# Optimization experiments

Hardware: AMD Instinct MI355X
Metric: run time of the kernel (lower is better)

The kernel has to match this reference:

```python
import jax, jax.numpy as jnp
import numpy as np

N_NODES = 100000
N_EDGES = 1600000
N_GRAPHS = 2000
N_FEAT = 128
HIDDEN = 128
N_LAYERS = 4
BN_EPS = 1e-5


def setup_inputs() -> dict:
    key = jax.random.key(0)
    ks = jax.random.split(key, 8)
    x = jax.random.normal(ks[0], (N_NODES, N_FEAT), dtype=jnp.float32)
    edge_index = jax.random.randint(ks[1], (2, N_EDGES), 0, N_NODES, dtype=jnp.int32)
    batch = jnp.sort(jax.random.randint(ks[2], (N_NODES,), 0, N_GRAPHS, dtype=jnp.int32))
    # layer weights scaled down to keep activations stable over 4 layers
    Ws = jax.random.normal(ks[3], (N_LAYERS, HIDDEN, HIDDEN), dtype=jnp.float32) * 0.1
    bs = jnp.zeros((N_LAYERS, HIDDEN), jnp.float32)
    gammas = jnp.ones((N_LAYERS, HIDDEN), jnp.float32)
    betas = jnp.zeros((N_LAYERS, HIDDEN), jnp.float32)
    run_mean = jnp.zeros((N_LAYERS, HIDDEN), jnp.float32)
    run_var = jnp.ones((N_LAYERS, HIDDEN), jnp.float32)
    W_out = jax.random.normal(ks[4], (HIDDEN, 5), dtype=jnp.float32) * 0.1
    b_out = jnp.zeros((5,), jnp.float32)
    return {"x": x, "edge_index": edge_index, "batch": batch, "Ws": Ws, "bs": bs,
            "gammas": gammas, "betas": betas, "run_mean": run_mean, "run_var": run_var,
            "W_out": W_out, "b_out": b_out}


def _gcn_conv(x, src, dst, norm, self_coef, W, b):
    xw = x @ W                                        # [N, H]
    coef = norm[src] * norm[dst]                      # [E]
    msgs = xw[src] * coef[:, None]                    # [E, H] gather
    agg = jax.ops.segment_sum(msgs, dst, num_segments=N_NODES)  # scatter-add
    agg = agg + xw * self_coef[:, None]               # self-loop term
    return agg + b


def reference(x, edge_index, batch, Ws, bs, gammas, betas, run_mean, run_var, W_out, b_out):
    src, dst = edge_index[0], edge_index[1]
    # degree (incl. self-loop) from destination index
    deg = jax.ops.segment_sum(jnp.ones((N_EDGES,), x.dtype), dst, num_segments=N_NODES) + 1.0
    norm = jax.lax.rsqrt(deg)
    self_coef = norm * norm
    h = x
    for l in range(N_LAYERS):
        h = _gcn_conv(h, src, dst, norm, self_coef, Ws[l], bs[l])
        # BatchNorm1d in eval mode (running stats); dropout is identity in eval
        h = (h - run_mean[l]) * (gammas[l] * jax.lax.rsqrt(run_var[l] + BN_EPS)) + betas[l]
        h = jax.nn.relu(h)
    # global mean pool over graphs
    sums = jax.ops.segment_sum(h, batch, num_segments=N_GRAPHS)
    counts = jax.ops.segment_sum(jnp.ones((N_NODES,), h.dtype), batch, num_segments=N_GRAPHS)
    pooled = sums / jnp.maximum(counts, 1.0)[:, None]  # [G, H]
    return pooled @ W_out + b_out                      # [G, 5]
```

## Files before the change

kernel.cpp:

```cpp
#include <hip/hip_runtime.h>
#include <hip/hip_fp16.h>

#define N_NODES_C 100000
#define N_EDGES_C 1600000
#define N_GRAPHS_C 2000
#define HID 128
#define BN_EPS_C 1e-5f
#define NBUCK 391
#define PART_TILE 4096

typedef _Float16 half8 __attribute__((ext_vector_type(8)));
typedef float float4v __attribute__((ext_vector_type(4)));


__global__ __launch_bounds__(256) void k_twhist(const float* __restrict__ Ws_all, _Float16* __restrict__ WT,
                                                const int* __restrict__ dst, int* __restrict__ bcount,
                                                _Float16* __restrict__ yB_dummy) {
    const int t = threadIdx.x;
    int idx = blockIdx.x * 256 + t;
    if (idx < 4 * HID * HID) {
        int l = idx >> 14, r = idx & 16383, k = r >> 7, n = r & 127;
        WT[l * 16384 + n * HID + k] = (_Float16)Ws_all[idx];
    }
    if (blockIdx.x == 390 && t < 64) ((int*)yB_dummy)[t] = 0;
    __shared__ int hist[NBUCK];
    for (int b = t; b < NBUCK; b += 256) hist[b] = 0;
    __syncthreads();
    const int e0 = blockIdx.x * PART_TILE;
    #pragma unroll
    for (int k = 0; k < 16; k++) {
        int e = e0 + k * 256 + t;
        if (e < N_EDGES_C) atomicAdd(&hist[dst[e] >> 8], 1);
    }
    __syncthreads();
    for (int b = t; b < NBUCK; b += 256) {
        int c = hist[b];
        if (c) atomicAdd(&bcount[b], c);
    }
}

__global__ __launch_bounds__(256) void kb_part(const int* __restrict__ src, const int* __restrict__ dst,
                                               const int* __restrict__ bcount, int* __restrict__ relcur,
                                               int* __restrict__ ebuf) {
    __shared__ int sb[512];
    __shared__ int hist[NBUCK];
    __shared__ int startA[NBUCK];
    __shared__ int lcur[NBUCK];
    const int t = threadIdx.x;
    int v0 = (t < NBUCK) ? bcount[t] : 0;
    int v1 = (t + 256 < NBUCK) ? bcount[t + 256] : 0;
    sb[t] = v0; sb[t + 256] = v1;
    for (int b = t; b < NBUCK; b += 256) { hist[b] = 0; lcur[b] = 0; }
    __syncthreads();
    for (int off = 1; off < 512; off <<= 1) {
        int a  = (t >= off) ? sb[t - off] : 0;
        int b2 = (t + 256 >= off) ? sb[t + 256 - off] : 0;
        __syncthreads();
        sb[t] += a; sb[t + 256] += b2;
        __syncthreads();
    }
    sb[t] -= v0; sb[t + 256] -= v1;
    __syncthreads();
    const int e0 = blockIdx.x * PART_TILE;
    #pragma unroll
    for (int k = 0; k < 16; k++) {
        int e = e0 + k * 256 + t;
        if (e < N_EDGES_C) atomicAdd(&hist[dst[e] >> 8], 1);
    }
    __syncthreads();
    for (int b = t; b < NBUCK; b += 256) {
        int c = hist[b];
        startA[b] = c ? (sb[b] + atomicAdd(&relcur[b], c)) : 0;
    }
    __syncthreads();
    #pragma unroll
    for (int k = 0; k < 16; k++) {
        int e = e0 + k * 256 + t;
        if (e < N_EDGES_C) {
            int d = dst[e];
            int b = d >> 8;
            int pos = startA[b] + atomicAdd(&lcur[b], 1);
            ebuf[pos] = (src[e] << 8) | (d & 255);
        }
    }
}

__global__ __launch_bounds__(256) void kb_fill(const int* __restrict__ ebuf, const int* __restrict__ bcount,
                                               int* __restrict__ csr_src, int* __restrict__ offs,
                                               float* __restrict__ norm) {
    __shared__ int sb[512];
    __shared__ int s[256];
    __shared__ int excl[256];
    __shared__ int lcur[256];
    const int b = blockIdx.x, t = threadIdx.x;
    int v0 = (t < NBUCK) ? bcount[t] : 0;
    int v1 = (t + 256 < NBUCK) ? bcount[t + 256] : 0;
    sb[t] = v0; sb[t + 256] = v1;
    s[t] = 0; lcur[t] = 0;
    __syncthreads();
    for (int off = 1; off < 512; off <<= 1) {
        int a  = (t >= off) ? sb[t - off] : 0;
        int b2 = (t + 256 >= off) ? sb[t + 256 - off] : 0;
        __syncthreads();
        sb[t] += a; sb[t + 256] += b2;
        __syncthreads();
    }
    sb[t] -= v0; sb[t + 256] -= v1;
    __syncthreads();
    const int base = b << 8;
    const int e0 = sb[b], e1 = sb[b] + bcount[b];
    for (int e = e0 + t; e < e1; e += 256)
        atomicAdd(&s[ebuf[e] & 255], 1);
    __syncthreads();
    int own = s[t];
    for (int off = 1; off < 256; off <<= 1) {
        int v = (t >= off) ? s[t - off] : 0;
        __syncthreads();
        s[t] += v;
        __syncthreads();
    }
    excl[t] = s[t] - own;
    int node = base + t;
    if (node < N_NODES_C) {
        offs[node] = e0 + (s[t] - own);
        norm[node] = rsqrtf((float)own + 1.0f);
    }
    if (b == 0 && t == 0) offs[N_NODES_C] = N_EDGES_C;
    __syncthreads();
    for (int e = e0 + t; e < e1; e += 256) {
        int p = ebuf[e];
        int l = p & 255;
        int pos = e0 + excl[l] + atomicAdd(&lcur[l], 1);
        csr_src[pos] = p >> 8;
    }
}


__global__ __launch_bounds__(256) void k_gemm0(const float* __restrict__ Ap,
                                               const _Float16* __restrict__ WT,
                                               const float* __restrict__ norm,
                                               _Float16* __restrict__ Y, int nrows) {
    __shared__ _Float16 Wt[HID][136];
    const int tid = threadIdx.x;
    #pragma unroll
    for (int t = 0; t < 8; t++) {
        int off = tid * 8 + t * 2048;
        *(half8*)&Wt[off >> 7][off & 127] = *(const half8*)&WT[off];
    }
    __syncthreads();

    const int wave = tid >> 6, lane = tid & 63, quad = lane >> 4, l16 = lane & 15;
    half8 Wf[2][4];
    #pragma unroll
    for (int c = 0; c < 2; c++)
        #pragma unroll
        for (int ks = 0; ks < 4; ks++)
            Wf[c][ks] = *(const half8*)&Wt[(wave * 2 + c) * 16 + l16][ks * 32 + quad * 8];

    const int nbase = blockIdx.x * 128;
    #pragma unroll
    for (int t = 0; t < 8; t++) {
        int node = nbase + t * 16 + l16;
        bool ok = node < nrows;
        half8 Af[4];
        const float* arow = Ap + (long)node * HID;
        #pragma unroll
        for (int ks = 0; ks < 4; ks++) {
            if (ok) {
                float4 fa = *(const float4*)&arow[ks * 32 + quad * 8];
                float4 fb = *(const float4*)&arow[ks * 32 + quad * 8 + 4];
                _Float16 pk[8] = {(_Float16)fa.x, (_Float16)fa.y, (_Float16)fa.z, (_Float16)fa.w,
                                  (_Float16)fb.x, (_Float16)fb.y, (_Float16)fb.z, (_Float16)fb.w};
                Af[ks] = *(half8*)pk;
            } else Af[ks] = half8{};
        }
        float4v a0 = {0.f, 0.f, 0.f, 0.f}, a1 = {0.f, 0.f, 0.f, 0.f};
        #pragma unroll
        for (int ks = 0; ks < 4; ks++) {
            a0 = __builtin_amdgcn_mfma_f32_16x16x32_f16(Wf[0][ks], Af[ks], a0, 0, 0, 0);
            a1 = __builtin_amdgcn_mfma_f32_16x16x32_f16(Wf[1][ks], Af[ks], a1, 0, 0, 0);
        }
        float nv = ok ? norm[node] : 0.f;
        _Float16 p0[4], p1[4];
        #pragma unroll
        for (int r = 0; r < 4; r++) {
            p0[r] = (_Float16)(a0[r] * nv);
            p1[r] = (_Float16)(a1[r] * nv);
        }
        *(ushort4*)&Y[(long)node * HID + (wave * 2 + 0) * 16 + quad * 4] = *(ushort4*)p0;
        *(ushort4*)&Y[(long)node * HID + (wave * 2 + 1) * 16 + quad * 4] = *(ushort4*)p1;
    }
}


template<bool LAST>
__global__ __launch_bounds__(512, 8) void k_fused(
    const __half* __restrict__ yin, _Float16* __restrict__ yout,
    const _Float16* __restrict__ WTn, const int* __restrict__ offs,
    const int* __restrict__ csr, const float* __restrict__ norm,
    const float* __restrict__ bias, const float* __restrict__ mean,
    const float* __restrict__ gam, const float* __restrict__ varr,
    const float* __restrict__ bet, const int* __restrict__ batch,
    float* __restrict__ psum, int* __restrict__ pcount)
{
    __shared__ __half ht[32][136];
    const int tid = threadIdx.x;
    const int wv = __builtin_amdgcn_readfirstlane(tid >> 6);
    const int lane = tid & 63;
    const int quad = lane >> 4, l16 = lane & 15;
    const int j = lane * 2;
    const int nbase = blockIdx.x * 32;

    half8 Wf[4];
    if constexpr (!LAST) {
        #pragma unroll
        for (int ks = 0; ks < 4; ks++)
            Wf[ks] = *(const half8*)&WTn[(long)(wv * 16 + l16) * HID + ks * 32 + quad * 8];
    }

    for (int r = 0; r < 4; r++) {
        const int li = wv * 4 + r;
        const int i = nbase + li;
        float2 f = __half22float2(*(const __half2*)&yin[(long)i * HID + j]);
        float acc0 = f.x, acc1 = f.y;
        const int e0 = offs[i], e1 = offs[i + 1];
        int e = e0;
        do {
            int id[16];
            #pragma unroll
            for (int u = 0; u < 16; u++) {
                int raw = csr[e + u];
                id[u] = (e + u < e1) ? raw : N_NODES_C;
            }
            #pragma unroll
            for (int u = 0; u < 16; u++) {
                float2 g2 = __half22float2(*(const __half2*)&yin[(long)id[u] * HID + j]);
                acc0 += g2.x; acc1 += g2.y;
            }
            e += 16;
        } while (e < e1);
        const float ni = norm[i];
        float2 bi = *(const float2*)&bias[j];
        float2 me = *(const float2*)&mean[j];
        float2 ga = *(const float2*)&gam[j];
        float2 va = *(const float2*)&varr[j];
        float2 be = *(const float2*)&bet[j];
        float v0 = (acc0 * ni + bi.x - me.x) * (ga.x * rsqrtf(va.x + BN_EPS_C)) + be.x;
        float v1 = (acc1 * ni + bi.y - me.y) * (ga.y * rsqrtf(va.y + BN_EPS_C)) + be.y;
        *(__half2*)&ht[li][j] = __floats2half2_rn(fmaxf(v0, 0.f), fmaxf(v1, 0.f));
    }
    __syncthreads();

    if constexpr (!LAST) {
        #pragma unroll
        for (int ng = 0; ng < 2; ng++) {
            half8 Af[4];
            #pragma unroll
            for (int ks = 0; ks < 4; ks++)
                Af[ks] = *(const half8*)&ht[ng * 16 + l16][ks * 32 + quad * 8];
            float4v a0 = {0.f, 0.f, 0.f, 0.f};
            #pragma unroll
            for (int ks = 0; ks < 4; ks++)
                a0 = __builtin_amdgcn_mfma_f32_16x16x32_f16(Wf[ks], Af[ks], a0, 0, 0, 0);
            const int node = nbase + ng * 16 + l16;
            const float nv = norm[node];
            _Float16 p[4];
            #pragma unroll
            for (int r = 0; r < 4; r++) p[r] = (_Float16)(a0[r] * nv);
            *(ushort4*)&yout[(long)node * HID + wv * 16 + quad * 4] = *(ushort4*)p;
        }
    } else {
        const int sub = tid >> 7, t7 = tid & 127;
        const int i0 = nbase + sub * 8, iend = i0 + 8;
        float acc = 0.f;
        int cur = batch[i0];
        int runStart = i0;
        for (int i = i0; i < iend; i++) {
            int g = batch[i];
            if (g != cur) {
                atomicAdd(&psum[(long)cur * HID + t7], acc);
                if (t7 == 0) atomicAdd(&pcount[cur], i - runStart);
                acc = 0.f; cur = g; runStart = i;
            }
            acc += __half2float(ht[i - nbase][t7]);
        }
        atomicAdd(&psum[(long)cur * HID + t7], acc);
        if (t7 == 0) atomicAdd(&pcount[cur], iend - runStart);
    }
}

__global__ __launch_bounds__(128) void k_final(const float* __restrict__ psum, const int* __restrict__ pcount,
                                               const float* __restrict__ W_out, const float* __restrict__ b_out,
                                               float* __restrict__ out) {
    __shared__ float red[128][5];
    const int g = blockIdx.x, j = threadIdx.x;
    float cnt = fmaxf((float)pcount[g], 1.f);
    float p = psum[(long)g * HID + j] / cnt;
    #pragma unroll
    for (int o = 0; o < 5; o++) red[j][o] = p * W_out[j * 5 + o];
    __syncthreads();
    for (int off = 64; off >= 1; off >>= 1) {
        if (j < off) {
            #pragma unroll
            for (int o = 0; o < 5; o++) red[j][o] += red[j + off][o];
        }
        __syncthreads();
    }
    if (j < 5) out[g * 5 + j] = red[0][j] + b_out[j];
}


extern "C" void kernel_launch(void* const* d_in, const int* in_sizes, int n_in,
                              void* d_out, int out_size, void* d_ws, size_t ws_size,
                              hipStream_t stream) {
    const float* x        = (const float*)d_in[0];
    const int*   eidx     = (const int*)d_in[1];
    const int*   src      = eidx;
    const int*   dst      = eidx + N_EDGES_C;
    const int*   batch    = (const int*)d_in[2];
    const float* Ws_all   = (const float*)d_in[3];
    const float* bs       = (const float*)d_in[4];
    const float* gammas   = (const float*)d_in[5];
    const float* betas    = (const float*)d_in[6];
    const float* run_mean = (const float*)d_in[7];
    const float* run_var  = (const float*)d_in[8];
    const float* W_out    = (const float*)d_in[9];
    const float* b_out    = (const float*)d_in[10];
    float* out = (float*)d_out;

    char* wp = (char*)d_ws;
    auto alloc = [&](size_t bytes) { char* p = wp; wp += (bytes + 255) & ~(size_t)255; return p; };
    _Float16* yA      = (_Float16*)alloc((size_t)(N_NODES_C + 128) * HID * 2);
    _Float16* yB      = (_Float16*)alloc((size_t)(N_NODES_C + 128) * HID * 2);
    int*      ebuf    = (int*)yA;
    _Float16* WT      = (_Float16*)alloc((size_t)4 * HID * HID * 2);
    int*      csr_src = (int*)alloc((size_t)(N_EDGES_C + 16) * 4);
    int*      offs    = (int*)alloc((size_t)(N_NODES_C + 1) * 4);
    float*    norm    = (float*)alloc((size_t)N_NODES_C * 4);
    char*     zbeg    = wp;
    float*    psum    = (float*)alloc((size_t)N_GRAPHS_C * HID * 4);
    int*      pcount  = (int*)alloc((size_t)N_GRAPHS_C * 4);
    int*      bcount  = (int*)alloc((NBUCK + 1) * 4);
    int*      relcur  = (int*)alloc((NBUCK + 1) * 4);
    size_t    zlen    = (size_t)(wp - zbeg);

    hipMemsetAsync(zbeg, 0, zlen, stream);

    const int PB = (N_EDGES_C + PART_TILE - 1) / PART_TILE;
    k_twhist<<<PB, 256, 0, stream>>>(Ws_all, WT, dst, bcount, yB + (size_t)N_NODES_C * HID);
    kb_part <<<PB, 256, 0, stream>>>(src, dst, bcount, relcur, ebuf);
    kb_fill <<<NBUCK, 256, 0, stream>>>(ebuf, bcount, csr_src, offs, norm);

    const int GB = (N_NODES_C + 127) / 128;
    const int FB = N_NODES_C / 32;
    k_gemm0<<<GB, 256, 0, stream>>>(x, WT, norm, yA, N_NODES_C);

    k_fused<false><<<FB, 512, 0, stream>>>((const __half*)yA, yB, WT + 1 * 16384, offs, csr_src, norm,
                                           bs + 0 * HID, run_mean + 0 * HID, gammas + 0 * HID,
                                           run_var + 0 * HID, betas + 0 * HID, nullptr, nullptr, nullptr);
    k_fused<false><<<FB, 512, 0, stream>>>((const __half*)yB, yA, WT + 2 * 16384, offs, csr_src, norm,
                                           bs + 1 * HID, run_mean + 1 * HID, gammas + 1 * HID,
                                           run_var + 1 * HID, betas + 1 * HID, nullptr, nullptr, nullptr);
    k_fused<false><<<FB, 512, 0, stream>>>((const __half*)yA, yB, WT + 3 * 16384, offs, csr_src, norm,
                                           bs + 2 * HID, run_mean + 2 * HID, gammas + 2 * HID,
                                           run_var + 2 * HID, betas + 2 * HID, nullptr, nullptr, nullptr);
    k_fused<true><<<FB, 512, 0, stream>>>((const __half*)yB, nullptr, nullptr, offs, csr_src, norm,
                                          bs + 3 * HID, run_mean + 3 * HID, gammas + 3 * HID,
                                          run_var + 3 * HID, betas + 3 * HID, batch, psum, pcount);

    k_final<<<N_GRAPHS_C, 128, 0, stream>>>(psum, pcount, W_out, b_out, out);
}
```

Measured before the change: 447.2 us.

## Fuse layer-0 GEMM into CSR fill kernel and move psum zeroing into histogram kernel

The first-layer x@W GEMM is merged into the CSR fill kernel. Each of the 391 bucket blocks computes the 256 nodes it owns, using norm values kept in shared memory, so one kernel launch and the norm reload go away. Zeroing of psum/pcount moves from the memset into k_twhist, which shrinks the memset, and ebuf is relocated to yB so that yA can be written during the fill. The cost is that the GEMM now runs on only 391 blocks with W fragments loaded directly from global memory, so it may be less parallel than the old 782-block GEMM.

```diff
diff --git a/kernel.cpp b/kernel.cpp
--- a/kernel.cpp
+++ b/kernel.cpp
@@ -15,8 +15,10 @@
 
 __global__ __launch_bounds__(256) void k_twhist(const float* __restrict__ Ws_all, _Float16* __restrict__ WT,
                                                 const int* __restrict__ dst, int* __restrict__ bcount,
-                                                _Float16* __restrict__ yB_dummy) {
+                                                _Float16* __restrict__ yB_dummy,
+                                                int* __restrict__ zp, int zn) {
     const int t = threadIdx.x;
+    for (int i = blockIdx.x * 256 + t; i < zn; i += gridDim.x * 256) zp[i] = 0;
     int idx = blockIdx.x * 256 + t;
     if (idx < 4 * HID * HID) {
         int l = idx >> 14, r = idx & 16383, k = r >> 7, n = r & 127;
@@ -85,14 +87,27 @@
     }
 }
 
-__global__ __launch_bounds__(256) void kb_fill(const int* __restrict__ ebuf, const int* __restrict__ bcount,
-                                               int* __restrict__ csr_src, int* __restrict__ offs,
-                                               float* __restrict__ norm) {
+
+__global__ __launch_bounds__(256) void kb_fillg(const int* __restrict__ ebuf, const int* __restrict__ bcount,
+                                                int* __restrict__ csr_src, int* __restrict__ offs,
+                                                float* __restrict__ norm,
+                                                const float* __restrict__ x, const _Float16* __restrict__ WT0,
+                                                _Float16* __restrict__ yA) {
     __shared__ int sb[512];
     __shared__ int s[256];
     __shared__ int excl[256];
     __shared__ int lcur[256];
+    __shared__ float nsh[256];
     const int b = blockIdx.x, t = threadIdx.x;
+    const int wave = t >> 6, lane = t & 63, quad = lane >> 4, l16 = lane & 15;
+
+    half8 Wf[2][4];
+    #pragma unroll
+    for (int c = 0; c < 2; c++)
+        #pragma unroll
+        for (int ks = 0; ks < 4; ks++)
+            Wf[c][ks] = *(const half8*)&WT0[(long)((wave * 2 + c) * 16 + l16) * HID + ks * 32 + quad * 8];
+
     int v0 = (t < NBUCK) ? bcount[t] : 0;
     int v1 = (t + 256 < NBUCK) ? bcount[t + 256] : 0;
     sb[t] = v0; sb[t + 256] = v1;
@@ -123,8 +138,10 @@
     int node = base + t;
     if (node < N_NODES_C) {
         offs[node] = e0 + (s[t] - own);
-        norm[node] = rsqrtf((float)own + 1.0f);
-    }
+        float nv = rsqrtf((float)own + 1.0f);
+        norm[node] = nv;
+        nsh[t] = nv;
+    } else nsh[t] = 0.f;
     if (b == 0 && t == 0) offs[N_NODES_C] = N_EDGES_C;
     __syncthreads();
     for (int e = e0 + t; e < e1; e += 256) {
@@ -133,62 +150,43 @@
         int pos = e0 + excl[l] + atomicAdd(&lcur[l], 1);
         csr_src[pos] = p >> 8;
     }
-}
-
-
-__global__ __launch_bounds__(256) void k_gemm0(const float* __restrict__ Ap,
-                                               const _Float16* __restrict__ WT,
-                                               const float* __restrict__ norm,
-                                               _Float16* __restrict__ Y, int nrows) {
-    __shared__ _Float16 Wt[HID][136];
-    const int tid = threadIdx.x;
-    #pragma unroll
-    for (int t = 0; t < 8; t++) {
-        int off = tid * 8 + t * 2048;
-        *(half8*)&Wt[off >> 7][off & 127] = *(const half8*)&WT[off];
-    }
-    __syncthreads();
-
-    const int wave = tid >> 6, lane = tid & 63, quad = lane >> 4, l16 = lane & 15;
-    half8 Wf[2][4];
-    #pragma unroll
-    for (int c = 0; c < 2; c++)
+    __syncthreads();
+
+    #pragma unroll
+    for (int tile = 0; tile < 2; tile++) {
+        const int nb2 = base + tile * 128;
         #pragma unroll
-        for (int ks = 0; ks < 4; ks++)
-            Wf[c][ks] = *(const half8*)&Wt[(wave * 2 + c) * 16 + l16][ks * 32 + quad * 8];
-
-    const int nbase = blockIdx.x * 128;
-    #pragma unroll
-    for (int t = 0; t < 8; t++) {
-        int node = nbase + t * 16 + l16;
-        bool ok = node < nrows;
-        half8 Af[4];
-        const float* arow = Ap + (long)node * HID;
-        #pragma unroll
-        for (int ks = 0; ks < 4; ks++) {
-            if (ok) {
-                float4 fa = *(const float4*)&arow[ks * 32 + quad * 8];
-                float4 fb = *(const float4*)&arow[ks * 32 + quad * 8 + 4];
-                _Float16 pk[8] = {(_Float16)fa.x, (_Float16)fa.y, (_Float16)fa.z, (_Float16)fa.w,
-                                  (_Float16)fb.x, (_Float16)fb.y, (_Float16)fb.z, (_Float16)fb.w};
-                Af[ks] = *(half8*)pk;
-            } else Af[ks] = half8{};
-        }
-        float4v a0 = {0.f, 0.f, 0.f, 0.f}, a1 = {0.f, 0.f, 0.f, 0.f};
-        #pragma unroll
-        for (int ks = 0; ks < 4; ks++) {
-            a0 = __builtin_amdgcn_mfma_f32_16x16x32_f16(Wf[0][ks], Af[ks], a0, 0, 0, 0);
-            a1 = __builtin_amdgcn_mfma_f32_16x16x32_f16(Wf[1][ks], Af[ks], a1, 0, 0, 0);
-        }
-        float nv = ok ? norm[node] : 0.f;
-        _Float16 p0[4], p1[4];
-        #pragma unroll
-        for (int r = 0; r < 4; r++) {
-            p0[r] = (_Float16)(a0[r] * nv);
-            p1[r] = (_Float16)(a1[r] * nv);
-        }
-        *(ushort4*)&Y[(long)node * HID + (wave * 2 + 0) * 16 + quad * 4] = *(ushort4*)p0;
-        *(ushort4*)&Y[(long)node * HID + (wave * 2 + 1) * 16 + quad * 4] = *(ushort4*)p1;
+        for (int tt = 0; tt < 8; tt++) {
+            int nd = nb2 + tt * 16 + l16;
+            bool ok = nd < N_NODES_C;
+            half8 Af[4];
+            const float* arow = x + (long)nd * HID;
+            #pragma unroll
+            for (int ks = 0; ks < 4; ks++) {
+                if (ok) {
+                    float4 fa = *(const float4*)&arow[ks * 32 + quad * 8];
+                    float4 fb = *(const float4*)&arow[ks * 32 + quad * 8 + 4];
+                    _Float16 pk[8] = {(_Float16)fa.x, (_Float16)fa.y, (_Float16)fa.z, (_Float16)fa.w,
+                                      (_Float16)fb.x, (_Float16)fb.y, (_Float16)fb.z, (_Float16)fb.w};
+                    Af[ks] = *(half8*)pk;
+                } else Af[ks] = half8{};
+            }
+            float4v a0 = {0.f, 0.f, 0.f, 0.f}, a1 = {0.f, 0.f, 0.f, 0.f};
+            #pragma unroll
+            for (int ks = 0; ks < 4; ks++) {
+                a0 = __builtin_amdgcn_mfma_f32_16x16x32_f16(Wf[0][ks], Af[ks], a0, 0, 0, 0);
+                a1 = __builtin_amdgcn_mfma_f32_16x16x32_f16(Wf[1][ks], Af[ks], a1, 0, 0, 0);
+            }
+            float nv = nsh[nd - base];
+            _Float16 p0[4], p1[4];
+            #pragma unroll
+            for (int r = 0; r < 4; r++) {
+                p0[r] = (_Float16)(a0[r] * nv);
+                p1[r] = (_Float16)(a1[r] * nv);
+            }
+            *(ushort4*)&yA[(long)nd * HID + (wave * 2 + 0) * 16 + quad * 4] = *(ushort4*)p0;
+            *(ushort4*)&yA[(long)nd * HID + (wave * 2 + 1) * 16 + quad * 4] = *(ushort4*)p1;
+        }
     }
 }
 
@@ -332,14 +330,14 @@
     auto alloc = [&](size_t bytes) { char* p = wp; wp += (bytes + 255) & ~(size_t)255; return p; };
     _Float16* yA      = (_Float16*)alloc((size_t)(N_NODES_C + 128) * HID * 2);
     _Float16* yB      = (_Float16*)alloc((size_t)(N_NODES_C + 128) * HID * 2);
-    int*      ebuf    = (int*)yA;
+    int*      ebuf    = (int*)yB;
     _Float16* WT      = (_Float16*)alloc((size_t)4 * HID * HID * 2);
     int*      csr_src = (int*)alloc((size_t)(N_EDGES_C + 16) * 4);
     int*      offs    = (int*)alloc((size_t)(N_NODES_C + 1) * 4);
     float*    norm    = (float*)alloc((size_t)N_NODES_C * 4);
-    char*     zbeg    = wp;
     float*    psum    = (float*)alloc((size_t)N_GRAPHS_C * HID * 4);
     int*      pcount  = (int*)alloc((size_t)N_GRAPHS_C * 4);
+    char*     zbeg    = wp;
     int*      bcount  = (int*)alloc((NBUCK + 1) * 4);
     int*      relcur  = (int*)alloc((NBUCK + 1) * 4);
     size_t    zlen    = (size_t)(wp - zbeg);
@@ -347,14 +345,13 @@
     hipMemsetAsync(zbeg, 0, zlen, stream);
 
     const int PB = (N_EDGES_C + PART_TILE - 1) / PART_TILE;
-    k_twhist<<<PB, 256, 0, stream>>>(Ws_all, WT, dst, bcount, yB + (size_t)N_NODES_C * HID);
+    const int ZN = N_GRAPHS_C * HID + N_GRAPHS_C;
+    k_twhist<<<PB, 256, 0, stream>>>(Ws_all, WT, dst, bcount, yB + (size_t)N_NODES_C * HID,
+                                     (int*)psum, ZN);
     kb_part <<<PB, 256, 0, stream>>>(src, dst, bcount, relcur, ebuf);
-    kb_fill <<<NBUCK, 256, 0, stream>>>(ebuf, bcount, csr_src, offs, norm);
-
-    const int GB = (N_NODES_C + 127) / 128;
+    kb_fillg<<<NBUCK, 256, 0, stream>>>(ebuf, bcount, csr_src, offs, norm, x, WT, yA);
+
     const int FB = N_NODES_C / 32;
-    k_gemm0<<<GB, 256, 0, stream>>>(x, WT, norm, yA, N_NODES_C);
-
     k_fused<false><<<FB, 512, 0, stream>>>((const __half*)yA, yB, WT + 1 * 16384, offs, csr_src, norm,
                                            bs + 0 * HID, run_mean + 0 * HID, gammas + 0 * HID,
                                            run_var + 0 * HID, betas + 0 * HID, nullptr, nullptr, nullptr);
```

Result: slower. 456.2 us (+2.0%).
